# Kernel tuning notes

Measured on AMD Instinct MI355X. Metric: run time of the kernel, lower is better.

The kernel has to match this reference:

```python
import jax, jax.numpy as jnp
import numpy as np

# NF4 (NormalFloat4) codebook from bitsandbytes
NF4 = jnp.array([
    -1.0, -0.6961928009986877, -0.5250730514526367, -0.39491748809814453,
    -0.28444138169288635, -0.18477343022823334, -0.09105003625154495, 0.0,
    0.07958029955625534, 0.16093020141124725, 0.24611230194568634,
    0.33791524171829224, 0.44070982933044434, 0.5626170039176941,
    0.7229568362236023, 1.0], dtype=jnp.float32)

BLOCK = 64          # bnb default quantization block size
RANK = 8
ALPHA = 16
SCALING = ALPHA / RANK


def setup_inputs() -> dict:
    key = jax.random.key(0)
    k = jax.random.split(key, 6)
    B, S, I, O = 4, 2048, 4096, 4096
    x = jax.random.normal(k[0], (B, S, I), dtype=jnp.float32)
    w_codes = jax.random.randint(k[1], (O, I), 0, 16, dtype=jnp.int32)
    absmax = jax.random.uniform(k[2], (O, I // BLOCK), dtype=jnp.float32)
    bias = jax.random.normal(k[3], (O,), dtype=jnp.float32)
    lora_A = jax.random.normal(k[4], (I, RANK), dtype=jnp.float32) / np.sqrt(I)
    lora_B = jax.random.normal(k[5], (RANK, O), dtype=jnp.float32)
    return {"x": x, "w_codes": w_codes, "absmax": absmax, "bias": bias,
            "lora_A": lora_A, "lora_B": lora_B}


def reference(x, w_codes, absmax, bias, lora_A, lora_B):
    O, I = w_codes.shape
    # NF4 dequantize: code lookup scaled by per-block absmax -> W [O, I]
    W = (NF4[w_codes].reshape(O, I // BLOCK, BLOCK) * absmax[:, :, None]).reshape(O, I)
    base = jnp.einsum('bsi,oi->bso', x, W) + bias
    # low-rank LoRA branch (dropout=0 -> identity)
    lora = ((x @ lora_A) @ lora_B) * SCALING
    return base + lora
```

## Files before the change

kernel.cpp:

```cpp
#include <hip/hip_runtime.h>
#include <hip/hip_bf16.h>
#include <stdint.h>


typedef __bf16 bf16x8 __attribute__((ext_vector_type(8)));
typedef float  f32x4  __attribute__((ext_vector_type(4)));
typedef unsigned short u16x8 __attribute__((ext_vector_type(8)));

__constant__ float NF4_TAB[16] = {
    -1.0f, -0.6961928009986877f, -0.5250730514526367f, -0.39491748809814453f,
    -0.28444138169288635f, -0.18477343022823334f, -0.09105003625154495f, 0.0f,
    0.07958029955625534f, 0.16093020141124725f, 0.24611230194568634f,
    0.33791524171829224f, 0.44070982933044434f, 0.5626170039176941f,
    0.7229568362236023f, 1.0f};

__device__ __forceinline__ unsigned short f2bf(float f) {
    unsigned int u = __float_as_uint(f);
    u += 0x7FFFu + ((u >> 16) & 1u);
    return (unsigned short)(u >> 16);
}

__global__ __launch_bounds__(256) void cvt_x_kernel(
    const float* __restrict__ x, unsigned short* __restrict__ xb, int n8) {
    int i = blockIdx.x * 256 + threadIdx.x;
    if (i >= n8) return;
    const float4* p = (const float4*)x + (long)i * 2;
    float4 a = p[0], b = p[1];
    u16x8 o;
    o[0] = f2bf(a.x); o[1] = f2bf(a.y); o[2] = f2bf(a.z); o[3] = f2bf(a.w);
    o[4] = f2bf(b.x); o[5] = f2bf(b.y); o[6] = f2bf(b.z); o[7] = f2bf(b.w);
    *((u16x8*)xb + i) = o;
}

__global__ __launch_bounds__(256) void build_w_kernel(
    const int* __restrict__ codes, const float* __restrict__ absmax,
    const float* __restrict__ lA, const float* __restrict__ lB,
    unsigned short* __restrict__ W, int O, int I) {
    const int o  = blockIdx.y;
    const int i0 = blockIdx.x * 2048 + threadIdx.x * 8;
    float bo[8];
#pragma unroll
    for (int r = 0; r < 8; ++r) bo[r] = lB[(long)r * O + o] * 2.0f;
    const long base = (long)o * I + i0;
    const int4* cp = (const int4*)(codes + base);
    int4 c0 = cp[0], c1 = cp[1];
    const float am = absmax[o * (I >> 6) + (i0 >> 6)];
    int cc[8] = {c0.x, c0.y, c0.z, c0.w, c1.x, c1.y, c1.z, c1.w};
    u16x8 ov;
#pragma unroll
    for (int j = 0; j < 8; ++j) {
        const float4* ap = (const float4*)(lA + (long)(i0 + j) * 8);
        float4 a0 = ap[0], a1 = ap[1];
        float w = NF4_TAB[cc[j] & 15] * am;
        w += a0.x * bo[0] + a0.y * bo[1] + a0.z * bo[2] + a0.w * bo[3]
           + a1.x * bo[4] + a1.y * bo[5] + a1.z * bo[6] + a1.w * bo[7];
        ov[j] = f2bf(w);
    }
    *(u16x8*)(W + base) = ov;
}

#define BM 256
#define BN 256
#define BK 64

#define GLOAD16(g, s) __builtin_amdgcn_global_load_lds(                     \
    (const __attribute__((address_space(1))) void*)(g),                     \
    (__attribute__((address_space(3))) void*)(s), 16, 0, 0)

#define STAGE(ptr, ldsbase) do {                                            \
    GLOAD16((ptr), (char*)(ldsbase) + ldsW);                                \
    GLOAD16((ptr) + SK, (char*)(ldsbase) + 8192 + ldsW); } while (0)

#define BAR() do { asm volatile("" ::: "memory");                           \
    __builtin_amdgcn_s_barrier(); asm volatile("" ::: "memory"); } while (0)

#define MFMA_QUAD(H, KQ, BREG)                                              \
    _Pragma("unroll") for (int mi = 0; mi < 4; ++mi)                        \
    _Pragma("unroll") for (int ni = 0; ni < 2; ++ni) {                      \
        acc[H][KQ][mi][ni] = __builtin_amdgcn_mfma_f32_16x16x32_bf16(       \
            a[mi][0], BREG[ni][0], acc[H][KQ][mi][ni], 0, 0, 0);            \
        acc[H][KQ][mi][ni] = __builtin_amdgcn_mfma_f32_16x16x32_bf16(       \
            a[mi][1], BREG[ni][1], acc[H][KQ][mi][ni], 0, 0, 0); }

__global__ __launch_bounds__(512, 2) void gemm_kernel(
    const unsigned short* __restrict__ A,
    const unsigned short* __restrict__ Bm,
    const float* __restrict__ bias,
    float* __restrict__ out, int M, int N, int K) {
    __shared__ char lds[2][65536];

    const int t = threadIdx.x;
    const int w = t >> 6, l = t & 63;
    const int wr = w >> 2, wc = w & 3;
    const long mB = (long)blockIdx.y * BM;
    const long nB = (long)blockIdx.x * BN;
    const int NT = K / BK;

    const int sRow = w * 8 + (l >> 3);
    const int sCol = ((l & 7) ^ (l >> 3)) << 3;
    const int ldsW = w * 1024;
    const long SK = 64L * K;
    const long HK = 128L * K;
    const unsigned short* gA = A  + (mB + sRow) * K + sCol;
    const unsigned short* gB = Bm + (nB + sRow) * K + sCol;

    const unsigned short* pA1 = gA + HK + BK;
    const unsigned short* pB1 = gB + HK + BK;
    const unsigned short* pA0 = gA + 2 * BK;
    const unsigned short* pB0 = gB + 2 * BK;

    const int fr = l & 15;
    const int aoff0 = fr * 128 + ((((l >> 4)) ^ (l & 7)) << 4);
    const int aoff1 = fr * 128 + (((4 + (l >> 4)) ^ (l & 7)) << 4);

    f32x4 acc[2][2][4][2];
#pragma unroll
    for (int h = 0; h < 2; ++h)
#pragma unroll
        for (int k = 0; k < 2; ++k)
#pragma unroll
            for (int mi = 0; mi < 4; ++mi)
#pragma unroll
                for (int ni = 0; ni < 2; ++ni)
                    acc[h][k][mi][ni] = (f32x4){0.f, 0.f, 0.f, 0.f};

    STAGE(gA,      lds[0] + 0);
    STAGE(gA + HK, lds[0] + 16384);
    STAGE(gB,      lds[0] + 32768);
    STAGE(gB + HK, lds[0] + 49152);
    STAGE(gA + BK, lds[1] + 0);
    STAGE(gB + BK, lds[1] + 32768);
    asm volatile("s_waitcnt vmcnt(4)" ::: "memory");
    BAR();

    bf16x8 a[4][2], b0[2][2], b1[2][2];

    for (int g = 0; g < NT; ++g) {
        char* cur = lds[g & 1];
        char* nxt = lds[(g & 1) ^ 1];
        const char* Ab = cur + wr * 8192;
        const char* Bb = cur + 32768 + wc * 4096;
        const bool st1 = (g + 1 < NT), st2 = (g + 2 < NT);

#pragma unroll
        for (int mi = 0; mi < 4; ++mi) {
            a[mi][0] = *(const bf16x8*)(Ab + mi * 2048 + aoff0);
            a[mi][1] = *(const bf16x8*)(Ab + mi * 2048 + aoff1);
        }
#pragma unroll
        for (int ni = 0; ni < 2; ++ni) {
            b0[ni][0] = *(const bf16x8*)(Bb + ni * 2048 + aoff0);
            b0[ni][1] = *(const bf16x8*)(Bb + ni * 2048 + aoff1);
        }
        if (st1) STAGE(pA1, nxt + 16384);
        BAR();
        __builtin_amdgcn_s_setprio(1);
        MFMA_QUAD(0, 0, b0);
        __builtin_amdgcn_s_setprio(0);

#pragma unroll
        for (int ni = 0; ni < 2; ++ni) {
            b1[ni][0] = *(const bf16x8*)(Bb + 16384 + ni * 2048 + aoff0);
            b1[ni][1] = *(const bf16x8*)(Bb + 16384 + ni * 2048 + aoff1);
        }
        if (st1) STAGE(pB1, nxt + 49152);
        BAR();
        __builtin_amdgcn_s_setprio(1);
        MFMA_QUAD(0, 1, b1);
        __builtin_amdgcn_s_setprio(0);

#pragma unroll
        for (int mi = 0; mi < 4; ++mi) {
            a[mi][0] = *(const bf16x8*)(Ab + 16384 + mi * 2048 + aoff0);
            a[mi][1] = *(const bf16x8*)(Ab + 16384 + mi * 2048 + aoff1);
        }
        if (st2) STAGE(pA0, cur + 0);
        BAR();
        __builtin_amdgcn_s_setprio(1);
        MFMA_QUAD(1, 0, b0);
        __builtin_amdgcn_s_setprio(0);

        if (st2) STAGE(pB0, cur + 32768);
        if (st2) { asm volatile("s_waitcnt vmcnt(4)" ::: "memory"); }
        else     { asm volatile("s_waitcnt vmcnt(0)" ::: "memory"); }
        BAR();
        __builtin_amdgcn_s_setprio(1);
        MFMA_QUAD(1, 1, b1);
        __builtin_amdgcn_s_setprio(0);

        pA1 += BK; pB1 += BK; pA0 += BK; pB0 += BK;
    }

    const int r4 = (l >> 4) * 4;
#pragma unroll
    for (int kq = 0; kq < 2; ++kq) {
        float bs[2];
#pragma unroll
        for (int ni = 0; ni < 2; ++ni)
            bs[ni] = bias[nB + kq * 128 + wc * 32 + ni * 16 + fr];
#pragma unroll
        for (int h = 0; h < 2; ++h)
#pragma unroll
            for (int mi = 0; mi < 4; ++mi)
#pragma unroll
                for (int r = 0; r < 4; ++r) {
                    long row = mB + h * 128 + wr * 64 + mi * 16 + r4 + r;
                    float* op = out + row * N + nB + kq * 128 + wc * 32 + fr;
#pragma unroll
                    for (int ni = 0; ni < 2; ++ni)
                        op[ni * 16] = acc[h][kq][mi][ni][r] + bs[ni];
                }
    }
}

__global__ void naive_kernel(const float* __restrict__ x, const int* __restrict__ codes,
                             const float* __restrict__ absmax, const float* __restrict__ bias,
                             const float* __restrict__ lA, const float* __restrict__ lB,
                             float* __restrict__ out, int M, int I, int O) {
    long idx = (long)blockIdx.x * 256 + threadIdx.x;
    if (idx >= (long)M * O) return;
    int o = (int)(idx % O);
    long m = idx / O;
    const float* xr = x + m * I;
    const int* cr = codes + (long)o * I;
    const float* ar = absmax + (long)o * (I >> 6);
    float acc = 0.f;
    float la[8] = {0, 0, 0, 0, 0, 0, 0, 0};
    for (int i = 0; i < I; ++i) {
        float xv = xr[i];
        acc += xv * NF4_TAB[cr[i] & 15] * ar[i >> 6];
        const float* av = lA + (long)i * 8;
#pragma unroll
        for (int r = 0; r < 8; ++r) la[r] += xv * av[r];
    }
    float lv = 0.f;
#pragma unroll
    for (int r = 0; r < 8; ++r) lv += la[r] * lB[(long)r * O + o];
    out[idx] = acc + bias[o] + 2.0f * lv;
}

extern "C" void kernel_launch(void* const* d_in, const int* in_sizes, int n_in,
                              void* d_out, int out_size, void* d_ws, size_t ws_size,
                              hipStream_t stream) {
    const float* x      = (const float*)d_in[0];
    const int*   codes  = (const int*)d_in[1];
    const float* absmax = (const float*)d_in[2];
    const float* bias   = (const float*)d_in[3];
    const float* lA     = (const float*)d_in[4];
    const float* lB     = (const float*)d_in[5];
    float* out = (float*)d_out;

    const int I = in_sizes[4] / 8;
    const int O = in_sizes[3];
    const int M = in_sizes[0] / I;
    const int K = I;

    const size_t need = (size_t)M * K * 2 + (size_t)O * K * 2;
    if (ws_size < need || (M % BM) || (O % BN) || (K % 2048) || (K / BK) < 2) {
        long tot = (long)M * O;
        naive_kernel<<<(int)((tot + 255) / 256), 256, 0, stream>>>(
            x, codes, absmax, bias, lA, lB, out, M, I, O);
        return;
    }

    unsigned short* xb = (unsigned short*)d_ws;
    unsigned short* wb = xb + (size_t)M * K;

    const int n8 = (M * K) / 8;
    cvt_x_kernel<<<(n8 + 255) / 256, 256, 0, stream>>>(x, xb, n8);
    dim3 gw(K / 2048, O);
    build_w_kernel<<<gw, 256, 0, stream>>>(codes, absmax, lA, lB, wb, O, K);
    dim3 grid(O / BN, M / BM);
    gemm_kernel<<<grid, 512, 0, stream>>>(xb, wb, bias, out, M, O, K);
}
```

Measured before the change: 350.4 us.

## Merge prep kernels, add XCD-aware tile swizzle, retune GEMM waitcnts

```diff
diff --git a/kernel.cpp b/kernel.cpp
--- a/kernel.cpp
+++ b/kernel.cpp
@@ -20,43 +20,44 @@
     return (unsigned short)(u >> 16);
 }
 
-__global__ __launch_bounds__(256) void cvt_x_kernel(
-    const float* __restrict__ x, unsigned short* __restrict__ xb, int n8) {
-    int i = blockIdx.x * 256 + threadIdx.x;
-    if (i >= n8) return;
-    const float4* p = (const float4*)x + (long)i * 2;
-    float4 a = p[0], b = p[1];
-    u16x8 o;
-    o[0] = f2bf(a.x); o[1] = f2bf(a.y); o[2] = f2bf(a.z); o[3] = f2bf(a.w);
-    o[4] = f2bf(b.x); o[5] = f2bf(b.y); o[6] = f2bf(b.z); o[7] = f2bf(b.w);
-    *((u16x8*)xb + i) = o;
-}
-
-__global__ __launch_bounds__(256) void build_w_kernel(
+__global__ __launch_bounds__(256) void prep_kernel(
+    const float* __restrict__ x, unsigned short* __restrict__ xb, int n8, int nCvt,
     const int* __restrict__ codes, const float* __restrict__ absmax,
     const float* __restrict__ lA, const float* __restrict__ lB,
-    unsigned short* __restrict__ W, int O, int I) {
-    const int o  = blockIdx.y;
-    const int i0 = blockIdx.x * 2048 + threadIdx.x * 8;
-    float bo[8];
-#pragma unroll
-    for (int r = 0; r < 8; ++r) bo[r] = lB[(long)r * O + o] * 2.0f;
-    const long base = (long)o * I + i0;
-    const int4* cp = (const int4*)(codes + base);
-    int4 c0 = cp[0], c1 = cp[1];
-    const float am = absmax[o * (I >> 6) + (i0 >> 6)];
-    int cc[8] = {c0.x, c0.y, c0.z, c0.w, c1.x, c1.y, c1.z, c1.w};
-    u16x8 ov;
-#pragma unroll
-    for (int j = 0; j < 8; ++j) {
-        const float4* ap = (const float4*)(lA + (long)(i0 + j) * 8);
-        float4 a0 = ap[0], a1 = ap[1];
-        float w = NF4_TAB[cc[j] & 15] * am;
-        w += a0.x * bo[0] + a0.y * bo[1] + a0.z * bo[2] + a0.w * bo[3]
-           + a1.x * bo[4] + a1.y * bo[5] + a1.z * bo[6] + a1.w * bo[7];
-        ov[j] = f2bf(w);
-    }
-    *(u16x8*)(W + base) = ov;
+    unsigned short* __restrict__ W, int O, int I, int nIb) {
+    if ((int)blockIdx.x < nCvt) {
+        int i = blockIdx.x * 256 + threadIdx.x;
+        if (i >= n8) return;
+        const float4* p = (const float4*)x + (long)i * 2;
+        float4 a = p[0], b = p[1];
+        u16x8 o;
+        o[0] = f2bf(a.x); o[1] = f2bf(a.y); o[2] = f2bf(a.z); o[3] = f2bf(a.w);
+        o[4] = f2bf(b.x); o[5] = f2bf(b.y); o[6] = f2bf(b.z); o[7] = f2bf(b.w);
+        *((u16x8*)xb + i) = o;
+    } else {
+        const int b2 = blockIdx.x - nCvt;
+        const int o  = b2 / nIb;
+        const int i0 = (b2 - o * nIb) * 2048 + threadIdx.x * 8;
+        float bo[8];
+#pragma unroll
+        for (int r = 0; r < 8; ++r) bo[r] = lB[(long)r * O + o] * 2.0f;
+        const long base = (long)o * I + i0;
+        const int4* cp = (const int4*)(codes + base);
+        int4 c0 = cp[0], c1 = cp[1];
+        const float am = absmax[o * (I >> 6) + (i0 >> 6)];
+        int cc[8] = {c0.x, c0.y, c0.z, c0.w, c1.x, c1.y, c1.z, c1.w};
+        u16x8 ov;
+#pragma unroll
+        for (int j = 0; j < 8; ++j) {
+            const float4* ap = (const float4*)(lA + (long)(i0 + j) * 8);
+            float4 a0 = ap[0], a1 = ap[1];
+            float w = NF4_TAB[cc[j] & 15] * am;
+            w += a0.x * bo[0] + a0.y * bo[1] + a0.z * bo[2] + a0.w * bo[3]
+               + a1.x * bo[4] + a1.y * bo[5] + a1.z * bo[6] + a1.w * bo[7];
+            ov[j] = f2bf(w);
+        }
+        *(u16x8*)(W + base) = ov;
+    }
 }
 
 #define BM 256
@@ -86,14 +87,30 @@
     const unsigned short* __restrict__ A,
     const unsigned short* __restrict__ Bm,
     const float* __restrict__ bias,
-    float* __restrict__ out, int M, int N, int K) {
+    float* __restrict__ out, int M, int N, int K, int gx, int gy) {
     __shared__ char lds[2][65536];
+
+    int bx, by;
+    {
+        const int bid = blockIdx.x;
+        if ((gx & 7) == 0 && (gy & 7) == 0 && ((gx >> 3) * (gy >> 3)) == 8) {
+            const int xcd = bid & 7, loc = bid >> 3;
+            const int cxs = gx >> 3;
+            const int cr = xcd / cxs, cc = xcd - cr * cxs;
+            by = cr * 8 + (loc >> 3);
+            bx = cc * 8 + (loc & 7);
+        } else if (((gx * gy) & 7) == 0) {
+            const int q = (gx * gy) >> 3;
+            const int id = (bid & 7) * q + (bid >> 3);
+            bx = id % gx; by = id / gx;
+        } else { bx = bid % gx; by = bid / gx; }
+    }
 
     const int t = threadIdx.x;
     const int w = t >> 6, l = t & 63;
     const int wr = w >> 2, wc = w & 3;
-    const long mB = (long)blockIdx.y * BM;
-    const long nB = (long)blockIdx.x * BN;
+    const long mB = (long)by * BM;
+    const long nB = (long)bx * BN;
     const int NT = K / BK;
 
     const int sRow = w * 8 + (l >> 3);
@@ -153,6 +170,7 @@
             b0[ni][1] = *(const bf16x8*)(Bb + ni * 2048 + aoff1);
         }
         if (st1) STAGE(pA1, nxt + 16384);
+        asm volatile("s_waitcnt vmcnt(6)" ::: "memory");
         BAR();
         __builtin_amdgcn_s_setprio(1);
         MFMA_QUAD(0, 0, b0);
@@ -181,7 +199,7 @@
         __builtin_amdgcn_s_setprio(0);
 
         if (st2) STAGE(pB0, cur + 32768);
-        if (st2) { asm volatile("s_waitcnt vmcnt(4)" ::: "memory"); }
+        if (st2) { asm volatile("s_waitcnt vmcnt(8)" ::: "memory"); }
         else     { asm volatile("s_waitcnt vmcnt(0)" ::: "memory"); }
         BAR();
         __builtin_amdgcn_s_setprio(1);
@@ -266,10 +284,12 @@
     unsigned short* xb = (unsigned short*)d_ws;
     unsigned short* wb = xb + (size_t)M * K;
 
-    const int n8 = (M * K) / 8;
-    cvt_x_kernel<<<(n8 + 255) / 256, 256, 0, stream>>>(x, xb, n8);
-    dim3 gw(K / 2048, O);
-    build_w_kernel<<<gw, 256, 0, stream>>>(codes, absmax, lA, lB, wb, O, K);
-    dim3 grid(O / BN, M / BM);
-    gemm_kernel<<<grid, 512, 0, stream>>>(xb, wb, bias, out, M, O, K);
-}
+    const int n8   = (M * K) / 8;
+    const int nCvt = (n8 + 255) / 256;
+    const int nIb  = K / 2048;
+    const int nPrep = nCvt + O * nIb;
+    prep_kernel<<<nPrep, 256, 0, stream>>>(x, xb, n8, nCvt,
+                                           codes, absmax, lA, lB, wb, O, K, nIb);
+    const int gx = O / BN, gy = M / BM;
+    gemm_kernel<<<gx * gy, 512, 0, stream>>>(xb, wb, bias, out, M, O, K, gx, gy);
+}
```

Measured after the change: 353.2 us. About the same (+0.8%).
